# Kernel tuning notes

Measured on AMD Instinct MI355X. Metric: run time of the kernel, lower is better.

Reference implementation:

```python
import jax, jax.numpy as jnp
import numpy as np
import math

B, S, D = 4, 2048, 768
H, DH = 12, 64  # num heads, head dim; H*DH == D


def setup_inputs() -> dict:
    key = jax.random.key(0)
    ks = jax.random.split(key, 10)
    q = jax.random.normal(ks[0], (B, S, D), jnp.float32)
    k = jax.random.normal(ks[1], (B, S, D), jnp.float32)
    v = jax.random.normal(ks[2], (B, S, D), jnp.float32)
    attention_mask = jax.random.bernoulli(ks[3], 0.1, (B, S, S))
    s = 1.0 / math.sqrt(D)
    # Linear weights stored as [in, out] so projection is x @ W + b
    Wq = jax.random.uniform(ks[4], (D, D), jnp.float32, -s, s)
    bq = jax.random.uniform(ks[5], (D,), jnp.float32, -s, s)
    Wk = jax.random.uniform(ks[6], (D, D), jnp.float32, -s, s)
    bk = jax.random.uniform(ks[7], (D,), jnp.float32, -s, s)
    Wv = jax.random.uniform(ks[8], (D, D), jnp.float32, -s, s)
    bv = jax.random.uniform(ks[9], (D,), jnp.float32, -s, s)
    return {"q": q, "k": k, "v": v, "attention_mask": attention_mask,
            "Wq": Wq, "bq": bq, "Wk": Wk, "bk": bk, "Wv": Wv, "bv": bv}


def _split_heads(x):
    # [B, S, D] -> [B, H, S, DH]
    return x.reshape(B, -1, H, DH).transpose(0, 2, 1, 3)


def reference(q, k, v, attention_mask, Wq, bq, Wk, bk, Wv, bv):
    Q = _split_heads(q @ Wq + bq)
    K = _split_heads(k @ Wk + bk)
    V = _split_heads(v @ Wv + bv)
    scores = jnp.einsum('bhqd,bhkd->bhqk', Q, K) / math.sqrt(DH)
    # masked_fill(mask, -1e9); 3-dim mask broadcasts over heads
    scores = jnp.where(attention_mask[:, None, :, :], -1.0e9, scores)
    probs = jax.nn.softmax(scores, axis=-1)
    ctx = jnp.einsum('bhqk,bhkd->bhqd', probs, V)
    ctx = ctx.transpose(0, 2, 1, 3).reshape(B, -1, H * DH)
    return ctx, probs
```

## Files before the change

kernel.cpp:

```cpp
#include <hip/hip_runtime.h>
#include <hip/hip_bf16.h>

#define BB 4
#define SS 2048
#define DD 768
#define HH 12

typedef unsigned short u16t;
typedef unsigned char  u8t;
typedef unsigned int   u32t;
typedef __attribute__((ext_vector_type(8)))  short bf16x8;
typedef __attribute__((ext_vector_type(4)))  float f32x4;

union FragU { bf16x8 v; ushort4 h[2]; uint4 u; u32t g[4]; };

__device__ __forceinline__ u16t f2bf(float f) {
  union { float fv; u32t u; } x; x.fv = f;
  u32t r = x.u + 0x7FFFu + ((x.u >> 16) & 1u);
  return (u16t)(r >> 16);
}

__device__ __forceinline__ u32t pkbf2(float a, float b) {
  __hip_bfloat162 h2 = __float22bfloat162_rn(make_float2(a, b));
  union { __hip_bfloat162 h; u32t u; } c; c.h = h2;
  return c.u;
}

__device__ __forceinline__ u32t pack4(u32t w) {
  return ((w & 0x01010101u) * 0x01020408u) >> 24;
}
__device__ __forceinline__ u32t pack16b(uint4 v) {
  return pack4(v.x) | (pack4(v.y) << 4) | (pack4(v.z) << 8) | (pack4(v.w) << 12);
}
__device__ __forceinline__ u32t pack_i4(int4 v) {
  return (v.x ? 1u : 0u) | ((v.y ? 1u : 0u) << 1) | ((v.z ? 1u : 0u) << 2) | ((v.w ? 1u : 0u) << 3);
}
__device__ __forceinline__ u32t pack_f4(float4 v) {
  return (v.x != 0.f ? 1u : 0u) | ((v.y != 0.f ? 1u : 0u) << 1) |
         ((v.z != 0.f ? 1u : 0u) << 2) | ((v.w != 0.f ? 1u : 0u) << 3);
}

__global__ void detect_kernel(const u32t* __restrict__ mp, int* __restrict__ flag)
{
  __shared__ int s_isb, s_isf;
  if (threadIdx.x == 0) { s_isb = 0; s_isf = 0; }
  __syncthreads();
  int isb = 0, isf = 0;
  for (int i = threadIdx.x; i < 16384; i += 256) {
    u32t v = mp[i];
    if ((v & 0xFF000000u) == 0x3F000000u) isf = 1;
    else if (v & 0xFFFFFF00u) isb = 1;
  }
  if (isb) atomicOr(&s_isb, 1);
  if (isf) atomicOr(&s_isf, 1);
  __syncthreads();
  if (threadIdx.x == 0) *flag = s_isf ? 2 : (s_isb ? 1 : 0);
}

__global__ __launch_bounds__(256)
void mask_pack_kernel(const void* __restrict__ msk, const int* __restrict__ flagp,
                      u32t* __restrict__ pm)
{
  const int gid = blockIdx.x * 256 + threadIdx.x;
  const int row = gid >> 6, c = gid & 63;
  const int fmt = *flagp;
  const size_t src = (size_t)(row >> 11) * SS * SS + (size_t)(row & 2047) * SS + c * 32;
  u32t bits;
  if (fmt == 1) {
    const uint4* s = (const uint4*)((const u8t*)msk + src);
    bits = pack16b(s[0]) | (pack16b(s[1]) << 16);
  } else if (fmt == 0) {
    const int4* s = (const int4*)((const int*)msk + src);
    bits = 0;
#pragma unroll
    for (int j = 0; j < 8; ++j) bits |= pack_i4(s[j]) << (j * 4);
  } else {
    const float4* s = (const float4*)((const float*)msk + src);
    bits = 0;
#pragma unroll
    for (int j = 0; j < 8; ++j) bits |= pack_f4(s[j]) << (j * 4);
  }
  pm[(size_t)row * 64 + c] = bits;
}

__device__ __forceinline__ void proj_tile_gemm(const float* __restrict__ X,
    const float* __restrict__ W, int m0, int n0, int t,
    u16t* __restrict__ Al, u16t* __restrict__ Bl, f32x4 acc[8])
{
  const int w = t >> 6, l = t & 63;
  const int lq = l & 15, lg = l >> 4;
  const int ar = t >> 2, ac = (t & 3) * 8;
  const int bn = (t & 15) * 8;

  for (int kk = 0; kk < DD; kk += 32) {
    {
      const float* s = X + (size_t)(m0 + ar) * DD + kk + ac;
      float4 f0 = *(const float4*)s;
      float4 f1 = *(const float4*)(s + 4);
      u16t* d = &Al[ar * 40 + ac];
      d[0] = f2bf(f0.x); d[1] = f2bf(f0.y); d[2] = f2bf(f0.z); d[3] = f2bf(f0.w);
      d[4] = f2bf(f1.x); d[5] = f2bf(f1.y); d[6] = f2bf(f1.z); d[7] = f2bf(f1.w);
    }
#pragma unroll
    for (int rep = 0; rep < 2; ++rep) {
      const int c = (t >> 4) + rep * 16;
      const float* s = W + (size_t)(kk + c) * DD + n0 + bn;
      float4 f0 = *(const float4*)s;
      float4 f1 = *(const float4*)(s + 4);
      float fv[8] = {f0.x, f0.y, f0.z, f0.w, f1.x, f1.y, f1.z, f1.w};
#pragma unroll
      for (int e = 0; e < 8; ++e) {
        const int n = bn + e;
        Bl[n * 40 + (c ^ (((n >> 3) & 3) * 8))] = f2bf(fv[e]);
      }
    }
    __syncthreads();
    FragU a;
    const int arow = w * 16 + lq;
    a.h[0] = *(const ushort4*)&Al[arow * 40 + 4 * lg];
    a.h[1] = *(const ushort4*)&Al[arow * 40 + 4 * lg + 16];
#pragma unroll
    for (int nt = 0; nt < 8; ++nt) {
      const int bcol = nt * 16 + lq;
      const int xb = ((bcol >> 3) & 3) * 8;
      FragU bfr;
      bfr.h[0] = *(const ushort4*)&Bl[bcol * 40 + ((4 * lg) ^ xb)];
      bfr.h[1] = *(const ushort4*)&Bl[bcol * 40 + ((4 * lg + 16) ^ xb)];
      acc[nt] = __builtin_amdgcn_mfma_f32_16x16x32_bf16(a.v, bfr.v, acc[nt], 0, 0, 0);
    }
    __syncthreads();
  }
}

__global__ __launch_bounds__(256)
void proj_qk_kernel(const float* __restrict__ X, const float* __restrict__ W,
                    const float* __restrict__ bias, u16t* __restrict__ out)
{
  __shared__ u16t Al[64 * 40];
  __shared__ u16t Bl[128 * 40];
  const int t = threadIdx.x;
  const int w = t >> 6, l = t & 63;
  const int lq = l & 15, lg = l >> 4;
  const int m0 = blockIdx.x * 64;
  const int n0 = blockIdx.y * 128;
  const int b = m0 >> 11;

  f32x4 acc[8];
#pragma unroll
  for (int i = 0; i < 8; ++i)
#pragma unroll
    for (int r = 0; r < 4; ++r) acc[i][r] = 0.f;

  proj_tile_gemm(X, W, m0, n0, t, Al, Bl, acc);

#pragma unroll
  for (int nt = 0; nt < 8; ++nt) {
    const int n = n0 + nt * 16 + lq;
    const int h = n >> 6, dh = n & 63;
    const float bb = bias[n];
#pragma unroll
    for (int r = 0; r < 4; ++r) {
      const int s = (m0 & 2047) + w * 16 + 4 * lg + r;
      out[((size_t)(b * HH + h) * SS + s) * 64 + dh] = f2bf(acc[nt][r] + bb);
    }
  }
}

__global__ __launch_bounds__(256)
void proj_v_kernel(const float* __restrict__ X, const float* __restrict__ W,
                   const float* __restrict__ bias, u16t* __restrict__ out)
{
  __shared__ u16t Al[64 * 40];
  __shared__ u16t Bl[128 * 40];
  __shared__ u16t Tl[128 * 72];
  const int t = threadIdx.x;
  const int w = t >> 6, l = t & 63;
  const int lq = l & 15, lg = l >> 4;
  const int m0 = blockIdx.x * 64;
  const int n0 = blockIdx.y * 128;
  const int b = m0 >> 11;

  f32x4 acc[8];
#pragma unroll
  for (int i = 0; i < 8; ++i)
#pragma unroll
    for (int r = 0; r < 4; ++r) acc[i][r] = 0.f;

  proj_tile_gemm(X, W, m0, n0, t, Al, Bl, acc);

#pragma unroll
  for (int nt = 0; nt < 8; ++nt) {
    const float bb = bias[n0 + nt * 16 + lq];
#pragma unroll
    for (int r = 0; r < 4; ++r)
      Tl[(nt * 16 + lq) * 72 + w * 16 + 4 * lg + r] = f2bf(acc[nt][r] + bb);
  }
  __syncthreads();

  const int rowl = t >> 1;
  const int half = t & 1;
  const int ncol = n0 + rowl;
  const int h = ncol >> 6, dh = ncol & 63;
  const int s = (m0 & 2047) + half * 32;
  u16t* dst = out + ((size_t)(b * HH + h) * 64 + dh) * SS + s;
#pragma unroll
  for (int i = 0; i < 4; ++i) {
    uint4 vv = *(const uint4*)&Tl[rowl * 72 + half * 32 + i * 8];
    *(uint4*)(dst + i * 8) = vv;
  }
}

__global__ __launch_bounds__(256, 4)
void attn_kernel(const u16t* __restrict__ Qh, const u16t* __restrict__ Kh,
                 const u16t* __restrict__ Vh, const u32t* __restrict__ pm,
                 float* __restrict__ ctx, float* __restrict__ probs)
{
  __shared__ u16t Kl[2][64 * 64];
  __shared__ u16t Vt[2][64 * 64];

  const int t = threadIdx.x;
  const int w = t >> 6, l = t & 63;
  const int lq = l & 15, lg = l >> 4;

  const int bid = (int)blockIdx.x;
  const int lid = (bid & 7) * 192 + (bid >> 3);
  const int bh = lid >> 5;
  const int qt = lid & 31;
  const int b = bh / HH;
  const int qbase = qt * 64 + w * 16;

  const u16t* qh = Qh + (size_t)bh * SS * 64;
  const u16t* kh = Kh + (size_t)bh * SS * 64;
  const u16t* vh = Vh + (size_t)bh * SS * 64;

  FragU bq_[2];
  {
    const u16t* qp = qh + (size_t)(qbase + lq) * 64;
#pragma unroll
    for (int ks = 0; ks < 2; ++ks) {
      bq_[ks].h[0] = *(const ushort4*)(qp + ks * 32 + 4 * lg);
      bq_[ks].h[1] = *(const ushort4*)(qp + ks * 32 + 4 * lg + 16);
    }
  }

  const u32t* mrow = pm + ((size_t)b * SS + qbase + lq) * 64;

  const float SC = 0.125f * 1.44269504f;
  const float B4 = 4.0f * 1.44269504f;

#define STAGE_K(kt_, buf_)                                                        \
  _Pragma("unroll")                                                               \
  for (int j = 0; j < 2; ++j) {                                                   \
    const int rr = (w * 2 + j) * 8 + (l >> 3);                                    \
    const u16t* gsrc = kh + (size_t)((kt_) * 64 + rr) * 64 + ((l & 7) ^ (l >> 3)) * 8; \
    __builtin_amdgcn_global_load_lds(                                             \
        (const __attribute__((address_space(1))) void*)gsrc,                      \
        (__attribute__((address_space(3))) void*)(&Kl[buf_][(w * 2 + j) * 512]),  \
        16, 0, 0);                                                                \
  }

#define STAGE_V(kt_, buf_)                                                        \
  _Pragma("unroll")                                                               \
  for (int j = 0; j < 2; ++j) {                                                   \
    const int dv = (w * 2 + j) * 8 + (l >> 3);                                    \
    const u16t* gsrc = vh + (size_t)dv * SS + (kt_) * 64 + ((l & 7) ^ (l >> 3)) * 8; \
    __builtin_amdgcn_global_load_lds(                                             \
        (const __attribute__((address_space(1))) void*)gsrc,                      \
        (__attribute__((address_space(3))) void*)(&Vt[buf_][(w * 2 + j) * 512]),  \
        16, 0, 0);                                                                \
  }

#define QKT_CHUNK(nt_, buf_, accv)                                                \
  {                                                                               \
    const int krow = (nt_) * 16 + lq;                                             \
    const int xr = (krow & 7) * 8;                                                \
    _Pragma("unroll")                                                             \
    for (int r = 0; r < 4; ++r) (accv)[r] = 0.f;                                  \
    _Pragma("unroll")                                                             \
    for (int ks = 0; ks < 2; ++ks) {                                              \
      FragU ak;                                                                   \
      ak.h[0] = *(const ushort4*)&Kl[buf_][krow * 64 + ((ks * 32 + 4 * lg) ^ xr)];\
      ak.h[1] = *(const ushort4*)&Kl[buf_][krow * 64 + ((ks * 32 + 4 * lg + 16) ^ xr)]; \
      (accv) = __builtin_amdgcn_mfma_f32_16x16x32_bf16(ak.v, bq_[ks].v, (accv), 0, 0, 0); \
    }                                                                             \
  }

  float ssum = 0.f;

  STAGE_K(0, 0)
  asm volatile("s_waitcnt vmcnt(0)" ::: "memory");
  __syncthreads();

  for (int kt = 0; kt < 32; ++kt) {
    const int cur = kt & 1;
    if (kt < 31) { STAGE_K(kt + 1, cur ^ 1) }
    else         { STAGE_K(0, cur ^ 1) STAGE_V(0, cur ^ 1) }
    const uint2 mw = *(const uint2*)(mrow + kt * 2);
#pragma unroll
    for (int nt = 0; nt < 4; ++nt) {
      f32x4 a;
      QKT_CHUNK(nt, cur, a)
      const u32t word = (nt < 2) ? mw.x : mw.y;
      const int sh = 16 * (nt & 1) + 4 * lg;
#pragma unroll
      for (int r = 0; r < 4; ++r) {
        float s = fmaf(a[r], SC, -B4);
        if ((word >> (sh + r)) & 1) s = -1.0e9f;
        ssum += __builtin_exp2f(s);
      }
    }
    asm volatile("s_waitcnt vmcnt(0)" ::: "memory");
    __syncthreads();
  }

  ssum += __shfl_xor(ssum, 16);
  ssum += __shfl_xor(ssum, 32);
  const float inv = 1.0f / ssum;

  f32x4 acco[4];
#pragma unroll
  for (int i = 0; i < 4; ++i)
#pragma unroll
    for (int r = 0; r < 4; ++r) acco[i][r] = 0.f;

  const size_t prow = ((size_t)bh * SS + qbase + lq) * SS;

  for (int kt = 0; kt < 32; ++kt) {
    const int cur = kt & 1;
    if (kt < 31) { STAGE_K(kt + 1, cur ^ 1) STAGE_V(kt + 1, cur ^ 1) }
    const uint2 mw = *(const uint2*)(mrow + kt * 2);

    f32x4 sc[4];
#pragma unroll
    for (int nt = 0; nt < 4; ++nt) {
      f32x4 a;
      QKT_CHUNK(nt, cur, a)
      const u32t word = (nt < 2) ? mw.x : mw.y;
      const int sh = 16 * (nt & 1) + 4 * lg;
#pragma unroll
      for (int r = 0; r < 4; ++r) {
        float s = fmaf(a[r], SC, -B4);
        if ((word >> (sh + r)) & 1) s = -1.0e9f;
        sc[nt][r] = __builtin_exp2f(s) * inv;
      }
    }

#pragma unroll
    for (int nt = 0; nt < 4; ++nt) {
      __builtin_nontemporal_store(sc[nt], (f32x4*)(probs + prow + kt * 64 + nt * 16 + 4 * lg));
    }

    FragU pf[2];
#pragma unroll
    for (int c = 0; c < 2; ++c) {
      pf[c].g[0] = pkbf2(sc[2 * c][0],     sc[2 * c][1]);
      pf[c].g[1] = pkbf2(sc[2 * c][2],     sc[2 * c][3]);
      pf[c].g[2] = pkbf2(sc[2 * c + 1][0], sc[2 * c + 1][1]);
      pf[c].g[3] = pkbf2(sc[2 * c + 1][2], sc[2 * c + 1][3]);
    }

    __builtin_amdgcn_s_setprio(1);
#pragma unroll
    for (int c = 0; c < 2; ++c) {
#pragma unroll
      for (int n0 = 0; n0 < 4; ++n0) {
        const int dv = n0 * 16 + lq;
        const int xv = (dv & 7) * 8;
        FragU bv;
        bv.h[0] = *(const ushort4*)&Vt[cur][dv * 64 + ((c * 32 + 4 * lg) ^ xv)];
        bv.h[1] = *(const ushort4*)&Vt[cur][dv * 64 + ((c * 32 + 4 * lg + 16) ^ xv)];
        acco[n0] = __builtin_amdgcn_mfma_f32_16x16x32_bf16(pf[c].v, bv.v, acco[n0], 0, 0, 0);
      }
    }
    __builtin_amdgcn_s_setprio(0);

    asm volatile("s_waitcnt vmcnt(0)" ::: "memory");
    __syncthreads();
  }

  {
    const int h = bh % HH;
    const size_t cbase = (size_t)(b * SS + qbase) * DD + h * 64;
#pragma unroll
    for (int n0 = 0; n0 < 4; ++n0)
#pragma unroll
      for (int r = 0; r < 4; ++r)
        ctx[cbase + (size_t)(4 * lg + r) * DD + n0 * 16 + lq] = acco[n0][r];
  }
#undef STAGE_K
#undef STAGE_V
#undef QKT_CHUNK
}

extern "C" void kernel_launch(void* const* d_in, const int* in_sizes, int n_in,
                              void* d_out, int out_size, void* d_ws, size_t ws_size,
                              hipStream_t stream)
{
  const float* q   = (const float*)d_in[0];
  const float* k   = (const float*)d_in[1];
  const float* v   = (const float*)d_in[2];
  const void*  msk = d_in[3];
  const float* Wq  = (const float*)d_in[4];
  const float* bq  = (const float*)d_in[5];
  const float* Wk  = (const float*)d_in[6];
  const float* bk  = (const float*)d_in[7];
  const float* Wv  = (const float*)d_in[8];
  const float* bv  = (const float*)d_in[9];
  (void)in_sizes; (void)n_in; (void)out_size; (void)ws_size;

  const size_t NE = (size_t)BB * SS * DD;
  u16t* Qb = (u16t*)d_ws;
  u16t* Kb = Qb + NE;
  u16t* Vb = Kb + NE;
  u32t* pm = (u32t*)(Vb + NE);
  int* flag = (int*)(pm + (size_t)BB * SS * 64);

  float* ctx   = (float*)d_out;
  float* probs = ctx + NE;

  detect_kernel<<<1, 256, 0, stream>>>((const u32t*)msk, flag);
  mask_pack_kernel<<<2048, 256, 0, stream>>>(msk, flag, pm);

  dim3 pg(BB * SS / 64, DD / 128);
  proj_qk_kernel<<<pg, 256, 0, stream>>>(q, Wq, bq, Qb);
  proj_qk_kernel<<<pg, 256, 0, stream>>>(k, Wk, bk, Kb);
  proj_v_kernel <<<pg, 256, 0, stream>>>(v, Wv, bv, Vb);

  attn_kernel<<<dim3(1536), 256, 0, stream>>>(Qb, Kb, Vb, pm, ctx, probs);
}
```

Baseline: 429.4 us.

## Pre-convert projection inputs to bf16 and triple-buffer attention K/V loads

Adds pre-pass kernels that convert q/k/v activations to bf16 and transpose-convert the weights, using the probs output buffer as scratch. The projection GEMM then streams bf16 tiles with direct global-to-LDS loads, double-buffered over K=64 steps. The attention kernel moves from a double-buffered to a triple-buffered K/V pipeline with partial vmcnt waits and lower occupancy (launch bounds 3). This is meant to cut fp32 conversion work inside the GEMM and hide load latency in attention, at the cost of extra kernel launches and a full extra pass over the activations.

```diff
diff --git a/kernel.cpp b/kernel.cpp
--- a/kernel.cpp
+++ b/kernel.cpp
@@ -5,6 +5,7 @@
 #define SS 2048
 #define DD 768
 #define HH 12
+#define NE 6291456
 
 typedef unsigned short u16t;
 typedef unsigned char  u8t;
@@ -83,61 +84,115 @@
   pm[(size_t)row * 64 + c] = bits;
 }
 
-__device__ __forceinline__ void proj_tile_gemm(const float* __restrict__ X,
-    const float* __restrict__ W, int m0, int n0, int t,
-    u16t* __restrict__ Al, u16t* __restrict__ Bl, f32x4 acc[8])
+__global__ __launch_bounds__(256)
+void cvt_x_kernel(const float* __restrict__ q, const float* __restrict__ k,
+                  const float* __restrict__ v, u16t* __restrict__ xb)
+{
+  const float* src = (blockIdx.y == 0) ? q : (blockIdx.y == 1) ? k : v;
+  u16t* dst = xb + (size_t)blockIdx.y * NE;
+  const size_t i = ((size_t)blockIdx.x * 256 + threadIdx.x) * 8;
+  float4 f0 = *(const float4*)(src + i);
+  float4 f1 = *(const float4*)(src + i + 4);
+  uint4 o;
+  o.x = pkbf2(f0.x, f0.y); o.y = pkbf2(f0.z, f0.w);
+  o.z = pkbf2(f1.x, f1.y); o.w = pkbf2(f1.z, f1.w);
+  *(uint4*)(dst + i) = o;
+}
+
+__global__ __launch_bounds__(256)
+void cvt_w_kernel(const float* __restrict__ Wq, const float* __restrict__ Wk,
+                  const float* __restrict__ Wv, u16t* __restrict__ Wt)
+{
+  __shared__ u16t T[64 * 72];
+  const int t = threadIdx.x;
+  const float* W = (blockIdx.z == 0) ? Wq : (blockIdx.z == 1) ? Wk : Wv;
+  u16t* wt = Wt + (size_t)blockIdx.z * DD * DD;
+  const int n0 = blockIdx.x * 64, k0 = blockIdx.y * 64;
+  const int r = t >> 2, cs = (t & 3) * 16;
+#pragma unroll
+  for (int i = 0; i < 4; ++i) {
+    float4 f = *(const float4*)(W + (size_t)(k0 + r) * DD + n0 + cs + i * 4);
+    T[(cs + i * 4 + 0) * 72 + r] = f2bf(f.x);
+    T[(cs + i * 4 + 1) * 72 + r] = f2bf(f.y);
+    T[(cs + i * 4 + 2) * 72 + r] = f2bf(f.z);
+    T[(cs + i * 4 + 3) * 72 + r] = f2bf(f.w);
+  }
+  __syncthreads();
+#pragma unroll
+  for (int i = 0; i < 2; ++i) {
+    uint4 vv = *(const uint4*)&T[r * 72 + cs + i * 8];
+    *(uint4*)(wt + (size_t)(n0 + r) * DD + k0 + cs + i * 8) = vv;
+  }
+}
+
+__device__ __forceinline__ void proj_core(const u16t* __restrict__ Xrow,
+    const u16t* __restrict__ Wrow, u16t* __restrict__ Ab, u16t* __restrict__ Bb,
+    int t, f32x4 acc[8])
 {
   const int w = t >> 6, l = t & 63;
   const int lq = l & 15, lg = l >> 4;
-  const int ar = t >> 2, ac = (t & 3) * 8;
-  const int bn = (t & 15) * 8;
-
-  for (int kk = 0; kk < DD; kk += 32) {
-    {
-      const float* s = X + (size_t)(m0 + ar) * DD + kk + ac;
-      float4 f0 = *(const float4*)s;
-      float4 f1 = *(const float4*)(s + 4);
-      u16t* d = &Al[ar * 40 + ac];
-      d[0] = f2bf(f0.x); d[1] = f2bf(f0.y); d[2] = f2bf(f0.z); d[3] = f2bf(f0.w);
-      d[4] = f2bf(f1.x); d[5] = f2bf(f1.y); d[6] = f2bf(f1.z); d[7] = f2bf(f1.w);
-    }
-#pragma unroll
-    for (int rep = 0; rep < 2; ++rep) {
-      const int c = (t >> 4) + rep * 16;
-      const float* s = W + (size_t)(kk + c) * DD + n0 + bn;
-      float4 f0 = *(const float4*)s;
-      float4 f1 = *(const float4*)(s + 4);
-      float fv[8] = {f0.x, f0.y, f0.z, f0.w, f1.x, f1.y, f1.z, f1.w};
-#pragma unroll
-      for (int e = 0; e < 8; ++e) {
-        const int n = bn + e;
-        Bl[n * 40 + (c ^ (((n >> 3) & 3) * 8))] = f2bf(fv[e]);
+  const int gr = l >> 3;
+  const int gc = ((l & 7) ^ (l >> 3)) * 8;
+
+#define PSTAGE_A(kk_, buf_)                                                       \
+  _Pragma("unroll")                                                               \
+  for (int j = 0; j < 2; ++j) {                                                   \
+    const int rr = (w * 2 + j) * 8 + gr;                                          \
+    const u16t* gsrc = Xrow + (size_t)rr * DD + (kk_) + gc;                       \
+    __builtin_amdgcn_global_load_lds(                                             \
+        (const __attribute__((address_space(1))) void*)gsrc,                      \
+        (__attribute__((address_space(3))) void*)(Ab + (buf_) * 4096 + (w * 2 + j) * 512), \
+        16, 0, 0);                                                                \
+  }
+#define PSTAGE_B(kk_, buf_)                                                       \
+  _Pragma("unroll")                                                               \
+  for (int j = 0; j < 4; ++j) {                                                   \
+    const int rr = (w * 4 + j) * 8 + gr;                                          \
+    const u16t* gsrc = Wrow + (size_t)rr * DD + (kk_) + gc;                       \
+    __builtin_amdgcn_global_load_lds(                                             \
+        (const __attribute__((address_space(1))) void*)gsrc,                      \
+        (__attribute__((address_space(3))) void*)(Bb + (buf_) * 8192 + (w * 4 + j) * 512), \
+        16, 0, 0);                                                                \
+  }
+
+  PSTAGE_A(0, 0)
+  PSTAGE_B(0, 0)
+  __syncthreads();
+
+  const int xa = (lq & 7) * 8;
+  for (int kki = 0; kki < 12; ++kki) {
+    const int buf = kki & 1;
+    if (kki < 11) { PSTAGE_A((kki + 1) * 64, buf ^ 1) PSTAGE_B((kki + 1) * 64, buf ^ 1) }
+    const int arow = w * 16 + lq;
+    FragU af[2];
+#pragma unroll
+    for (int ks = 0; ks < 2; ++ks) {
+      af[ks].h[0] = *(const ushort4*)&Ab[buf * 4096 + arow * 64 + ((ks * 32 + 4 * lg) ^ xa)];
+      af[ks].h[1] = *(const ushort4*)&Ab[buf * 4096 + arow * 64 + ((ks * 32 + 4 * lg + 16) ^ xa)];
+    }
+#pragma unroll
+    for (int nt = 0; nt < 8; ++nt) {
+      const int brow = nt * 16 + lq;
+#pragma unroll
+      for (int ks = 0; ks < 2; ++ks) {
+        FragU bf;
+        bf.h[0] = *(const ushort4*)&Bb[buf * 8192 + brow * 64 + ((ks * 32 + 4 * lg) ^ xa)];
+        bf.h[1] = *(const ushort4*)&Bb[buf * 8192 + brow * 64 + ((ks * 32 + 4 * lg + 16) ^ xa)];
+        acc[nt] = __builtin_amdgcn_mfma_f32_16x16x32_bf16(af[ks].v, bf.v, acc[nt], 0, 0, 0);
       }
     }
     __syncthreads();
-    FragU a;
-    const int arow = w * 16 + lq;
-    a.h[0] = *(const ushort4*)&Al[arow * 40 + 4 * lg];
-    a.h[1] = *(const ushort4*)&Al[arow * 40 + 4 * lg + 16];
-#pragma unroll
-    for (int nt = 0; nt < 8; ++nt) {
-      const int bcol = nt * 16 + lq;
-      const int xb = ((bcol >> 3) & 3) * 8;
-      FragU bfr;
-      bfr.h[0] = *(const ushort4*)&Bl[bcol * 40 + ((4 * lg) ^ xb)];
-      bfr.h[1] = *(const ushort4*)&Bl[bcol * 40 + ((4 * lg + 16) ^ xb)];
-      acc[nt] = __builtin_amdgcn_mfma_f32_16x16x32_bf16(a.v, bfr.v, acc[nt], 0, 0, 0);
-    }
-    __syncthreads();
-  }
-}
-
-__global__ __launch_bounds__(256)
-void proj_qk_kernel(const float* __restrict__ X, const float* __restrict__ W,
+  }
+#undef PSTAGE_A
+#undef PSTAGE_B
+}
+
+__global__ __launch_bounds__(256, 3)
+void proj_qk_kernel(const u16t* __restrict__ Xb, const u16t* __restrict__ Wt,
                     const float* __restrict__ bias, u16t* __restrict__ out)
 {
-  __shared__ u16t Al[64 * 40];
-  __shared__ u16t Bl[128 * 40];
+  __shared__ u16t Ab[2 * 4096];
+  __shared__ u16t Bb[2 * 8192];
   const int t = threadIdx.x;
   const int w = t >> 6, l = t & 63;
   const int lq = l & 15, lg = l >> 4;
@@ -151,7 +206,7 @@
 #pragma unroll
     for (int r = 0; r < 4; ++r) acc[i][r] = 0.f;
 
-  proj_tile_gemm(X, W, m0, n0, t, Al, Bl, acc);
+  proj_core(Xb + (size_t)m0 * DD, Wt + (size_t)n0 * DD, Ab, Bb, t, acc);
 
 #pragma unroll
   for (int nt = 0; nt < 8; ++nt) {
@@ -166,13 +221,12 @@
   }
 }
 
-__global__ __launch_bounds__(256)
-void proj_v_kernel(const float* __restrict__ X, const float* __restrict__ W,
+__global__ __launch_bounds__(256, 3)
+void proj_v_kernel(const u16t* __restrict__ Xb, const u16t* __restrict__ Wt,
                    const float* __restrict__ bias, u16t* __restrict__ out)
 {
-  __shared__ u16t Al[64 * 40];
-  __shared__ u16t Bl[128 * 40];
-  __shared__ u16t Tl[128 * 72];
+  __shared__ u16t Ab[2 * 4096];
+  __shared__ u16t Bb[2 * 8192];
   const int t = threadIdx.x;
   const int w = t >> 6, l = t & 63;
   const int lq = l & 15, lg = l >> 4;
@@ -186,8 +240,9 @@
 #pragma unroll
     for (int r = 0; r < 4; ++r) acc[i][r] = 0.f;
 
-  proj_tile_gemm(X, W, m0, n0, t, Al, Bl, acc);
-
+  proj_core(Xb + (size_t)m0 * DD, Wt + (size_t)n0 * DD, Ab, Bb, t, acc);
+
+  u16t* Tl = Bb;
 #pragma unroll
   for (int nt = 0; nt < 8; ++nt) {
     const float bb = bias[n0 + nt * 16 + lq];
@@ -210,13 +265,13 @@
   }
 }
 
-__global__ __launch_bounds__(256, 4)
+__global__ __launch_bounds__(256, 3)
 void attn_kernel(const u16t* __restrict__ Qh, const u16t* __restrict__ Kh,
                  const u16t* __restrict__ Vh, const u32t* __restrict__ pm,
                  float* __restrict__ ctx, float* __restrict__ probs)
 {
-  __shared__ u16t Kl[2][64 * 64];
-  __shared__ u16t Vt[2][64 * 64];
+  __shared__ u16t Kb3[3][64 * 64];
+  __shared__ u16t Vb3[3][64 * 64];
 
   const int t = threadIdx.x;
   const int w = t >> 6, l = t & 63;
@@ -248,39 +303,42 @@
   const float SC = 0.125f * 1.44269504f;
   const float B4 = 4.0f * 1.44269504f;
 
+  const int gr = l >> 3;
+  const int gc = ((l & 7) ^ (l >> 3)) * 8;
+
 #define STAGE_K(kt_, buf_)                                                        \
   _Pragma("unroll")                                                               \
   for (int j = 0; j < 2; ++j) {                                                   \
-    const int rr = (w * 2 + j) * 8 + (l >> 3);                                    \
-    const u16t* gsrc = kh + (size_t)((kt_) * 64 + rr) * 64 + ((l & 7) ^ (l >> 3)) * 8; \
+    const int rr = (w * 2 + j) * 8 + gr;                                          \
+    const u16t* gsrc = kh + (size_t)((kt_) * 64 + rr) * 64 + gc;                  \
     __builtin_amdgcn_global_load_lds(                                             \
         (const __attribute__((address_space(1))) void*)gsrc,                      \
-        (__attribute__((address_space(3))) void*)(&Kl[buf_][(w * 2 + j) * 512]),  \
+        (__attribute__((address_space(3))) void*)(&Kb3[buf_][(w * 2 + j) * 512]), \
         16, 0, 0);                                                                \
   }
 
 #define STAGE_V(kt_, buf_)                                                        \
   _Pragma("unroll")                                                               \
   for (int j = 0; j < 2; ++j) {                                                   \
-    const int dv = (w * 2 + j) * 8 + (l >> 3);                                    \
-    const u16t* gsrc = vh + (size_t)dv * SS + (kt_) * 64 + ((l & 7) ^ (l >> 3)) * 8; \
+    const int dv = (w * 2 + j) * 8 + gr;                                          \
+    const u16t* gsrc = vh + (size_t)dv * SS + (kt_) * 64 + gc;                    \
     __builtin_amdgcn_global_load_lds(                                             \
         (const __attribute__((address_space(1))) void*)gsrc,                      \
-        (__attribute__((address_space(3))) void*)(&Vt[buf_][(w * 2 + j) * 512]),  \
+        (__attribute__((address_space(3))) void*)(&Vb3[buf_][(w * 2 + j) * 512]), \
         16, 0, 0);                                                                \
   }
 
 #define QKT_CHUNK(nt_, buf_, accv)                                                \
   {                                                                               \
     const int krow = (nt_) * 16 + lq;                                             \
-    const int xr = (krow & 7) * 8;                                                \
+    const int xr = (lq & 7) * 8;                                                  \
     _Pragma("unroll")                                                             \
     for (int r = 0; r < 4; ++r) (accv)[r] = 0.f;                                  \
     _Pragma("unroll")                                                             \
     for (int ks = 0; ks < 2; ++ks) {                                              \
       FragU ak;                                                                   \
-      ak.h[0] = *(const ushort4*)&Kl[buf_][krow * 64 + ((ks * 32 + 4 * lg) ^ xr)];\
-      ak.h[1] = *(const ushort4*)&Kl[buf_][krow * 64 + ((ks * 32 + 4 * lg + 16) ^ xr)]; \
+      ak.h[0] = *(const ushort4*)&Kb3[buf_][krow * 64 + ((ks * 32 + 4 * lg) ^ xr)]; \
+      ak.h[1] = *(const ushort4*)&Kb3[buf_][krow * 64 + ((ks * 32 + 4 * lg + 16) ^ xr)]; \
       (accv) = __builtin_amdgcn_mfma_f32_16x16x32_bf16(ak.v, bq_[ks].v, (accv), 0, 0, 0); \
     }                                                                             \
   }
@@ -288,18 +346,18 @@
   float ssum = 0.f;
 
   STAGE_K(0, 0)
-  asm volatile("s_waitcnt vmcnt(0)" ::: "memory");
-  __syncthreads();
-
+  STAGE_K(1, 1)
   for (int kt = 0; kt < 32; ++kt) {
-    const int cur = kt & 1;
-    if (kt < 31) { STAGE_K(kt + 1, cur ^ 1) }
-    else         { STAGE_K(0, cur ^ 1) STAGE_V(0, cur ^ 1) }
+    if (kt == 31) { asm volatile("s_waitcnt vmcnt(0)" ::: "memory"); }
+    else          { asm volatile("s_waitcnt vmcnt(2)" ::: "memory"); }
+    __builtin_amdgcn_s_barrier();
+    if (kt < 30) { STAGE_K(kt + 2, (kt + 2) % 3) }
+    const int buf = kt % 3;
     const uint2 mw = *(const uint2*)(mrow + kt * 2);
 #pragma unroll
     for (int nt = 0; nt < 4; ++nt) {
       f32x4 a;
-      QKT_CHUNK(nt, cur, a)
+      QKT_CHUNK(nt, buf, a)
       const u32t word = (nt < 2) ? mw.x : mw.y;
       const int sh = 16 * (nt & 1) + 4 * lg;
 #pragma unroll
@@ -309,8 +367,6 @@
         ssum += __builtin_exp2f(s);
       }
     }
-    asm volatile("s_waitcnt vmcnt(0)" ::: "memory");
-    __syncthreads();
   }
 
   ssum += __shfl_xor(ssum, 16);
@@ -325,16 +381,24 @@
 
   const size_t prow = ((size_t)bh * SS + qbase + lq) * SS;
 
+  __builtin_amdgcn_s_barrier();
+  STAGE_K(0, 0) STAGE_V(0, 0)
+  STAGE_K(1, 1) STAGE_V(1, 1)
+
   for (int kt = 0; kt < 32; ++kt) {
-    const int cur = kt & 1;
-    if (kt < 31) { STAGE_K(kt + 1, cur ^ 1) STAGE_V(kt + 1, cur ^ 1) }
+    if (kt == 0)                  { asm volatile("s_waitcnt vmcnt(4)"  ::: "memory"); }
+    else if (kt == 1 || kt == 31) { asm volatile("s_waitcnt vmcnt(8)"  ::: "memory"); }
+    else                          { asm volatile("s_waitcnt vmcnt(12)" ::: "memory"); }
+    __builtin_amdgcn_s_barrier();
+    if (kt < 30) { STAGE_K(kt + 2, (kt + 2) % 3) STAGE_V(kt + 2, (kt + 2) % 3) }
+    const int buf = kt % 3;
     const uint2 mw = *(const uint2*)(mrow + kt * 2);
 
     f32x4 sc[4];
 #pragma unroll
     for (int nt = 0; nt < 4; ++nt) {
       f32x4 a;
-      QKT_CHUNK(nt, cur, a)
+      QKT_CHUNK(nt, buf, a)
       const u32t word = (nt < 2) ? mw.x : mw.y;
       const int sh = 16 * (nt & 1) + 4 * lg;
 #pragma unroll
@@ -365,17 +429,14 @@
 #pragma unroll
       for (int n0 = 0; n0 < 4; ++n0) {
         const int dv = n0 * 16 + lq;
-        const int xv = (dv & 7) * 8;
+        const int xv = (lq & 7) * 8;
         FragU bv;
-        bv.h[0] = *(const ushort4*)&Vt[cur][dv * 64 + ((c * 32 + 4 * lg) ^ xv)];
-        bv.h[1] = *(const ushort4*)&Vt[cur][dv * 64 + ((c * 32 + 4 * lg + 16) ^ xv)];
+        bv.h[0] = *(const ushort4*)&Vb3[buf][dv * 64 + ((c * 32 + 4 * lg) ^ xv)];
+        bv.h[1] = *(const ushort4*)&Vb3[buf][dv * 64 + ((c * 32 + 4 * lg + 16) ^ xv)];
         acco[n0] = __builtin_amdgcn_mfma_f32_16x16x32_bf16(pf[c].v, bv.v, acco[n0], 0, 0, 0);
       }
     }
     __builtin_amdgcn_s_setprio(0);
-
-    asm volatile("s_waitcnt vmcnt(0)" ::: "memory");
-    __syncthreads();
   }
 
   {
@@ -408,7 +469,6 @@
   const float* bv  = (const float*)d_in[9];
   (void)in_sizes; (void)n_in; (void)out_size; (void)ws_size;
 
-  const size_t NE = (size_t)BB * SS * DD;
   u16t* Qb = (u16t*)d_ws;
   u16t* Kb = Qb + NE;
   u16t* Vb = Kb + NE;
@@ -418,13 +478,19 @@
   float* ctx   = (float*)d_out;
   float* probs = ctx + NE;
 
+  u16t* Xb = (u16t*)probs;
+  u16t* Wt = Xb + (size_t)3 * NE;
+
   detect_kernel<<<1, 256, 0, stream>>>((const u32t*)msk, flag);
   mask_pack_kernel<<<2048, 256, 0, stream>>>(msk, flag, pm);
 
+  cvt_x_kernel<<<dim3(3072, 3), 256, 0, stream>>>(q, k, v, Xb);
+  cvt_w_kernel<<<dim3(12, 12, 3), 256, 0, stream>>>(Wq, Wk, Wv, Wt);
+
   dim3 pg(BB * SS / 64, DD / 128);
-  proj_qk_kernel<<<pg, 256, 0, stream>>>(q, Wq, bq, Qb);
-  proj_qk_kernel<<<pg, 256, 0, stream>>>(k, Wk, bk, Kb);
-  proj_v_kernel <<<pg, 256, 0, stream>>>(v, Wv, bv, Vb);
+  proj_qk_kernel<<<pg, 256, 0, stream>>>(Xb,          Wt,               bq, Qb);
+  proj_qk_kernel<<<pg, 256, 0, stream>>>(Xb + NE,     Wt + DD * DD,     bk, Kb);
+  proj_v_kernel <<<pg, 256, 0, stream>>>(Xb + 2 * NE, Wt + 2 * DD * DD, bv, Vb);
 
   attn_kernel<<<dim3(1536), 256, 0, stream>>>(Qb, Kb, Vb, pm, ctx, probs);
 }
```

After: 415.5 us. 1.03x faster.
